# Kernel optimization log

Hardware: AMD Instinct MI355X
Metric: run time of the kernel (lower is better)

Reference implementation:

```python
import jax, jax.numpy as jnp
import numpy as np

VOCAB_SIZE = 1024
EMBED_DIM = 64
Z_SHAPE = (64, 32, 32, EMBED_DIM)


def setup_inputs() -> dict:
    key = jax.random.key(0)
    kz, kc = jax.random.split(key)
    z = jax.random.normal(kz, Z_SHAPE, dtype=jnp.float32)
    codebook = jax.random.uniform(kc, (VOCAB_SIZE, EMBED_DIM), dtype=jnp.float32)
    return {"z": z, "codebook": codebook}


def reference(z, codebook):
    # Flatten all leading dims: [N, D]
    z_flat = jnp.reshape(z, (-1, EMBED_DIM))
    # Squared euclidean distance via expansion: |z|^2 + |c|^2 - 2 z.c
    d1 = jnp.sum(z_flat ** 2, axis=1, keepdims=True)      # [N, 1]
    d2 = jnp.sum(codebook ** 2, axis=1)                   # [V]
    d3 = 2.0 * jnp.dot(z_flat, codebook.T)                # [N, V]
    distances = d1 + d2 - d3                              # [N, V]
    tokens = jnp.argmin(distances, axis=1)                # [N]
    tokens = jnp.reshape(tokens, z.shape[:-1])            # [B, H, W]
    z_quantized = codebook[tokens]                        # [B, H, W, D]
    return (z_quantized, tokens, codebook)
```

## Files before the change

### kernel.cpp

```cpp
#include <hip/hip_runtime.h>
#include <float.h>

constexpr int D     = 64;
constexpr int V     = 1024;
constexpr int NROWS = 65536;
constexpr float MARGIN = 0.01f;

typedef _Float16 half8 __attribute__((ext_vector_type(8)));
typedef float    f32x4 __attribute__((ext_vector_type(4)));

__global__ __launch_bounds__(256) void vq_prep(
    const float* __restrict__ cb, _Float16* __restrict__ wsH,
    _Float16* __restrict__ wsL, float* __restrict__ c2,
    float* __restrict__ cbout, int* __restrict__ cnt) {
  const int gid = blockIdx.x * 256 + threadIdx.x;
  if (gid == 0) cnt[0] = 0;

  ((float4*)cbout)[gid] = ((const float4*)cb)[gid];

  if (gid < V) {
    const int cw = gid;
    const float* src = cb + (size_t)cw * D;
    float part = 0.f;
#pragma unroll
    for (int chunk = 0; chunk < 8; ++chunk) {
      float4 q0 = ((const float4*)(src + chunk * 8))[0];
      float4 q1 = ((const float4*)(src + chunk * 8))[1];
      float xs[8] = {q0.x, q0.y, q0.z, q0.w, q1.x, q1.y, q1.z, q1.w};
      half8 hh, hl;
#pragma unroll
      for (int e = 0; e < 8; ++e) {
        _Float16 hi = (_Float16)xs[e];
        hh[e] = hi;
        hl[e] = (_Float16)(xs[e] - (float)hi);
        part  = fmaf(xs[e], xs[e], part);
      }
      *(half8*)&wsH[((size_t)chunk * V + cw) * 8] = hh;
      *(half8*)&wsL[((size_t)chunk * V + cw) * 8] = hl;
    }
    c2[cw] = part;
  }
}

__global__ __launch_bounds__(256, 4) void vq_screen(
    const float* __restrict__ z, const float* __restrict__ cb,
    const _Float16* __restrict__ wsH, const _Float16* __restrict__ wsL,
    const float* __restrict__ c2g,
    float* __restrict__ zq, float* __restrict__ tok,
    int* __restrict__ cnt, int* __restrict__ list) {
  __shared__ __align__(16) _Float16 sBh[8][128][8];
  __shared__ __align__(16) _Float16 sBl[8][128][8];
  __shared__ __align__(16) float sC2[128];
  __shared__ int   sW[4][16];
  __shared__ int   sFlagRows[64];
  __shared__ int   sFlagCnt, sFlagBase;

  const int tid  = threadIdx.x;
  const int lane = tid & 63;
  const int wv   = tid >> 6;
  const int l15  = lane & 15;
  const int quad = lane >> 4;
  const int gw   = blockIdx.x * 4 + wv;
  const int rowbase = gw * 16;

  if (tid == 0) sFlagCnt = 0;

  half8 afh[2], afl[2];
  {
    const float* zr = z + (size_t)(rowbase + l15) * D;
#pragma unroll
    for (int h = 0; h < 2; ++h) {
      const float4* p = (const float4*)(zr + h * 32 + quad * 8);
      float4 q0 = p[0], q1 = p[1];
      float xs[8] = {q0.x, q0.y, q0.z, q0.w, q1.x, q1.y, q1.z, q1.w};
      half8 ah, al;
#pragma unroll
      for (int e = 0; e < 8; ++e) {
        _Float16 hi = (_Float16)xs[e];
        ah[e] = hi;
        al[e] = (_Float16)(xs[e] - (float)hi);
      }
      afh[h] = ah; afl[h] = al;
    }
  }

  float b1[4], b2[4]; int i1[4];
#pragma unroll
  for (int r = 0; r < 4; ++r) { b1[r] = FLT_MAX; b2[r] = FLT_MAX; i1[r] = 0; }

  for (int phase = 0; phase < 8; ++phase) {
    __syncthreads();
#pragma unroll
    for (int i = 0; i < 8; ++i) {
      const int idx   = i * 256 + tid;
      const int seg   = idx >> 7;
      const int off   = idx & 127;
      const int chunk = seg & 7;
      const _Float16* srcb = (seg < 8) ? wsH : wsL;
      const half8 v = *(const half8*)&srcb[((size_t)chunk * V + phase * 128 + off) * 8];
      if (seg < 8) *(half8*)&sBh[chunk][off][0] = v;
      else         *(half8*)&sBl[chunk][off][0] = v;
    }
    if (tid < 32) {
      float4 q = ((const float4*)(c2g + phase * 128))[tid];
      *(float4*)&sC2[tid * 4] = q;
    }
    __syncthreads();
#pragma unroll 2
    for (int tl = 0; tl < 8; ++tl) {
      const int cwl  = tl * 16 + l15;
      const int vcol = phase * 128 + cwl;
      const float c2v = sC2[cwl];
      half8 bh0 = *(const half8*)&sBh[quad][cwl][0];
      half8 bh1 = *(const half8*)&sBh[4 + quad][cwl][0];
      half8 bl0 = *(const half8*)&sBl[quad][cwl][0];
      half8 bl1 = *(const half8*)&sBl[4 + quad][cwl][0];
      f32x4 acc = {0.f, 0.f, 0.f, 0.f};
      acc = __builtin_amdgcn_mfma_f32_16x16x32_f16(afh[0], bh0, acc, 0, 0, 0);
      acc = __builtin_amdgcn_mfma_f32_16x16x32_f16(afh[1], bh1, acc, 0, 0, 0);
      acc = __builtin_amdgcn_mfma_f32_16x16x32_f16(afh[0], bl0, acc, 0, 0, 0);
      acc = __builtin_amdgcn_mfma_f32_16x16x32_f16(afh[1], bl1, acc, 0, 0, 0);
      acc = __builtin_amdgcn_mfma_f32_16x16x32_f16(afl[0], bh0, acc, 0, 0, 0);
      acc = __builtin_amdgcn_mfma_f32_16x16x32_f16(afl[1], bh1, acc, 0, 0, 0);
#pragma unroll
      for (int r = 0; r < 4; ++r) {
        float m0 = fmaf(-2.f, acc[r], c2v);
        bool  c0 = m0 < b1[r];
        b2[r] = fminf(b2[r], fmaxf(m0, b1[r]));
        b1[r] = c0 ? m0 : b1[r];
        i1[r] = c0 ? vcol : i1[r];
      }
    }
  }

#pragma unroll
  for (int r = 0; r < 4; ++r) {
    float v1 = b1[r], v2 = b2[r]; int ix = i1[r];
#pragma unroll
    for (int s = 1; s < 16; s <<= 1) {
      float ov1 = __shfl_xor(v1, s);
      float ov2 = __shfl_xor(v2, s);
      int   oix = __shfl_xor(ix, s);
      bool take = (ov1 < v1) || (ov1 == v1 && oix < ix);
      float worse = take ? v1 : ov1;
      v2 = fminf(fminf(v2, ov2), worse);
      v1 = take ? ov1 : v1;
      ix = take ? oix : ix;
    }
    b1[r] = v1; b2[r] = v2; i1[r] = ix;
  }

  if (l15 == 0) {
#pragma unroll
    for (int r = 0; r < 4; ++r) {
      int rl = quad * 4 + r;
      sW[wv][rl] = i1[r];
      if (b2[r] - b1[r] < MARGIN) {
        int s = atomicAdd(&sFlagCnt, 1);
        sFlagRows[s] = rowbase + rl;
      }
    }
  }
  __syncthreads();
  if (tid == 0 && sFlagCnt > 0) sFlagBase = atomicAdd(cnt, sFlagCnt);
  __syncthreads();
  if (tid < sFlagCnt) list[sFlagBase + tid] = sFlagRows[tid];

  if (tid < 64) tok[blockIdx.x * 64 + tid] = (float)sW[tid >> 4][tid & 15];

#pragma unroll
  for (int i = 0; i < 4; ++i) {
    int cid = i * 256 + tid;
    int r = cid >> 4, seg = cid & 15;
    int widx = sW[r >> 4][r & 15];
    float4 val = *(const float4*)(cb + (size_t)widx * D + seg * 4);
    *(float4*)(zq + (size_t)(blockIdx.x * 64 + r) * D + seg * 4) = val;
  }
}

__global__ __launch_bounds__(256) void vq_fallback(
    const float* __restrict__ z, const float* __restrict__ cb,
    const int* __restrict__ cnt, const int* __restrict__ list,
    float* __restrict__ zq, float* __restrict__ tok) {
  __shared__ float sv[256];
  __shared__ int   si[256];
  const int t = threadIdx.x;
  const int n = cnt[0];
  for (int it = blockIdx.x; it < n; it += gridDim.x) {
    int row = __builtin_amdgcn_readfirstlane(list[it]);
    const float* zr = z + (size_t)row * D;
    float zreg[D];
#pragma unroll
    for (int i = 0; i < D / 4; ++i) {
      float4 q = ((const float4*)zr)[i];
      zreg[4 * i] = q.x; zreg[4 * i + 1] = q.y; zreg[4 * i + 2] = q.z; zreg[4 * i + 3] = q.w;
    }
    float d1 = 0.f;
#pragma unroll
    for (int i = 0; i < D; ++i) d1 = fmaf(zreg[i], zreg[i], d1);
    float best = FLT_MAX; int bidx = 0;
    for (int c = 0; c < 4; ++c) {
      int v = t + 256 * c;
      const float* cp = cb + (size_t)v * D;
      float acc = 0.f, cc = 0.f;
#pragma unroll
      for (int dd = 0; dd < D; ++dd) {
        acc = fmaf(zreg[dd], cp[dd], acc);
        cc  = fmaf(cp[dd], cp[dd], cc);
      }
      float dist = (d1 + cc) - 2.f * acc;
      if (dist < best) { best = dist; bidx = v; }
    }
    sv[t] = best; si[t] = bidx;
    __syncthreads();
    for (int s = 128; s > 0; s >>= 1) {
      if (t < s) {
        float v2 = sv[t + s]; int i2 = si[t + s];
        if (v2 < sv[t] || (v2 == sv[t] && i2 < si[t])) { sv[t] = v2; si[t] = i2; }
      }
      __syncthreads();
    }
    int win = si[0];
    if (t == 0) tok[row] = (float)win;
    if (t < 16) {
      float4 q = ((const float4*)(cb + (size_t)win * D))[t];
      ((float4*)(zq + (size_t)row * D))[t] = q;
    }
    __syncthreads();
  }
}

extern "C" void kernel_launch(void* const* d_in, const int* in_sizes, int n_in,
                              void* d_out, int out_size, void* d_ws, size_t ws_size,
                              hipStream_t stream) {
  const float* z  = (const float*)d_in[0];
  const float* cb = (const float*)d_in[1];

  float* out = (float*)d_out;
  float* zq  = out;
  float* tok = out + (size_t)NROWS * D;
  float* cbo = tok + NROWS;

  char* wsb = (char*)d_ws;
  _Float16* wsH  = (_Float16*)(wsb + 0);
  _Float16* wsL  = (_Float16*)(wsb + 131072);
  float*    c2   = (float*)(wsb + 262144);
  int*      cnt  = (int*)(wsb + 266240);
  int*      list = (int*)(wsb + 266496);

  vq_prep<<<64, 256, 0, stream>>>(cb, wsH, wsL, c2, cbo, cnt);
  vq_screen<<<1024, 256, 0, stream>>>(z, cb, wsH, wsL, c2, zq, tok, cnt, list);
  vq_fallback<<<1024, 256, 0, stream>>>(z, cb, cnt, list, zq, tok);
}
```

Baseline: 128.8 us.

## Process two 16-row tiles per wave to reuse staged codebook fragments

Each wave now handles 32 rows (two 16-row MFMA tiles) and reuses every codebook fragment loaded from shared memory for both tiles. The grid is halved to 512 blocks. This halves the global-to-LDS codebook staging and the LDS reads per row, at the cost of more registers per thread and fewer blocks to spread across the GPU.

```diff
diff --git a/kernel.cpp b/kernel.cpp
--- a/kernel.cpp
+++ b/kernel.cpp
@@ -51,8 +51,8 @@
   __shared__ __align__(16) _Float16 sBh[8][128][8];
   __shared__ __align__(16) _Float16 sBl[8][128][8];
   __shared__ __align__(16) float sC2[128];
-  __shared__ int   sW[4][16];
-  __shared__ int   sFlagRows[64];
+  __shared__ int   sW[4][32];
+  __shared__ int   sFlagRows[128];
   __shared__ int   sFlagCnt, sFlagBase;
 
   const int tid  = threadIdx.x;
@@ -61,13 +61,14 @@
   const int l15  = lane & 15;
   const int quad = lane >> 4;
   const int gw   = blockIdx.x * 4 + wv;
-  const int rowbase = gw * 16;
+  const int rowbase = gw * 32;
 
   if (tid == 0) sFlagCnt = 0;
 
-  half8 afh[2], afl[2];
-  {
-    const float* zr = z + (size_t)(rowbase + l15) * D;
+  half8 afh[2][2], afl[2][2];
+#pragma unroll
+  for (int rt = 0; rt < 2; ++rt) {
+    const float* zr = z + (size_t)(rowbase + rt * 16 + l15) * D;
 #pragma unroll
     for (int h = 0; h < 2; ++h) {
       const float4* p = (const float4*)(zr + h * 32 + quad * 8);
@@ -80,13 +81,15 @@
         ah[e] = hi;
         al[e] = (_Float16)(xs[e] - (float)hi);
       }
-      afh[h] = ah; afl[h] = al;
-    }
-  }
-
-  float b1[4], b2[4]; int i1[4];
-#pragma unroll
-  for (int r = 0; r < 4; ++r) { b1[r] = FLT_MAX; b2[r] = FLT_MAX; i1[r] = 0; }
+      afh[rt][h] = ah; afl[rt][h] = al;
+    }
+  }
+
+  float b1[2][4], b2[2][4]; int i1[2][4];
+#pragma unroll
+  for (int rt = 0; rt < 2; ++rt)
+#pragma unroll
+    for (int r = 0; r < 4; ++r) { b1[rt][r] = FLT_MAX; b2[rt][r] = FLT_MAX; i1[rt][r] = 0; }
 
   for (int phase = 0; phase < 8; ++phase) {
     __syncthreads();
@@ -115,27 +118,32 @@
       half8 bh1 = *(const half8*)&sBh[4 + quad][cwl][0];
       half8 bl0 = *(const half8*)&sBl[quad][cwl][0];
       half8 bl1 = *(const half8*)&sBl[4 + quad][cwl][0];
-      f32x4 acc = {0.f, 0.f, 0.f, 0.f};
-      acc = __builtin_amdgcn_mfma_f32_16x16x32_f16(afh[0], bh0, acc, 0, 0, 0);
-      acc = __builtin_amdgcn_mfma_f32_16x16x32_f16(afh[1], bh1, acc, 0, 0, 0);
-      acc = __builtin_amdgcn_mfma_f32_16x16x32_f16(afh[0], bl0, acc, 0, 0, 0);
-      acc = __builtin_amdgcn_mfma_f32_16x16x32_f16(afh[1], bl1, acc, 0, 0, 0);
-      acc = __builtin_amdgcn_mfma_f32_16x16x32_f16(afl[0], bh0, acc, 0, 0, 0);
-      acc = __builtin_amdgcn_mfma_f32_16x16x32_f16(afl[1], bh1, acc, 0, 0, 0);
-#pragma unroll
-      for (int r = 0; r < 4; ++r) {
-        float m0 = fmaf(-2.f, acc[r], c2v);
-        bool  c0 = m0 < b1[r];
-        b2[r] = fminf(b2[r], fmaxf(m0, b1[r]));
-        b1[r] = c0 ? m0 : b1[r];
-        i1[r] = c0 ? vcol : i1[r];
-      }
-    }
-  }
-
+#pragma unroll
+      for (int rt = 0; rt < 2; ++rt) {
+        f32x4 acc = {0.f, 0.f, 0.f, 0.f};
+        acc = __builtin_amdgcn_mfma_f32_16x16x32_f16(afh[rt][0], bh0, acc, 0, 0, 0);
+        acc = __builtin_amdgcn_mfma_f32_16x16x32_f16(afh[rt][1], bh1, acc, 0, 0, 0);
+        acc = __builtin_amdgcn_mfma_f32_16x16x32_f16(afh[rt][0], bl0, acc, 0, 0, 0);
+        acc = __builtin_amdgcn_mfma_f32_16x16x32_f16(afh[rt][1], bl1, acc, 0, 0, 0);
+        acc = __builtin_amdgcn_mfma_f32_16x16x32_f16(afl[rt][0], bh0, acc, 0, 0, 0);
+        acc = __builtin_amdgcn_mfma_f32_16x16x32_f16(afl[rt][1], bh1, acc, 0, 0, 0);
+#pragma unroll
+        for (int r = 0; r < 4; ++r) {
+          float m0 = fmaf(-2.f, acc[r], c2v);
+          bool  c0 = m0 < b1[rt][r];
+          b2[rt][r] = fminf(b2[rt][r], fmaxf(m0, b1[rt][r]));
+          b1[rt][r] = c0 ? m0 : b1[rt][r];
+          i1[rt][r] = c0 ? vcol : i1[rt][r];
+        }
+      }
+    }
+  }
+
+#pragma unroll
+  for (int rt = 0; rt < 2; ++rt)
 #pragma unroll
   for (int r = 0; r < 4; ++r) {
-    float v1 = b1[r], v2 = b2[r]; int ix = i1[r];
+    float v1 = b1[rt][r], v2 = b2[rt][r]; int ix = i1[rt][r];
 #pragma unroll
     for (int s = 1; s < 16; s <<= 1) {
       float ov1 = __shfl_xor(v1, s);
@@ -147,15 +155,17 @@
       v1 = take ? ov1 : v1;
       ix = take ? oix : ix;
     }
-    b1[r] = v1; b2[r] = v2; i1[r] = ix;
+    b1[rt][r] = v1; b2[rt][r] = v2; i1[rt][r] = ix;
   }
 
   if (l15 == 0) {
 #pragma unroll
+    for (int rt = 0; rt < 2; ++rt)
+#pragma unroll
     for (int r = 0; r < 4; ++r) {
-      int rl = quad * 4 + r;
-      sW[wv][rl] = i1[r];
-      if (b2[r] - b1[r] < MARGIN) {
+      int rl = rt * 16 + quad * 4 + r;
+      sW[wv][rl] = i1[rt][r];
+      if (b2[rt][r] - b1[rt][r] < MARGIN) {
         int s = atomicAdd(&sFlagCnt, 1);
         sFlagRows[s] = rowbase + rl;
       }
@@ -166,15 +176,15 @@
   __syncthreads();
   if (tid < sFlagCnt) list[sFlagBase + tid] = sFlagRows[tid];
 
-  if (tid < 64) tok[blockIdx.x * 64 + tid] = (float)sW[tid >> 4][tid & 15];
-
-#pragma unroll
-  for (int i = 0; i < 4; ++i) {
+  if (tid < 128) tok[blockIdx.x * 128 + tid] = (float)sW[tid >> 5][tid & 31];
+
+#pragma unroll
+  for (int i = 0; i < 8; ++i) {
     int cid = i * 256 + tid;
     int r = cid >> 4, seg = cid & 15;
-    int widx = sW[r >> 4][r & 15];
+    int widx = sW[r >> 5][r & 31];
     float4 val = *(const float4*)(cb + (size_t)widx * D + seg * 4);
-    *(float4*)(zq + (size_t)(blockIdx.x * 64 + r) * D + seg * 4) = val;
+    *(float4*)(zq + (size_t)(blockIdx.x * 128 + r) * D + seg * 4) = val;
   }
 }
 
@@ -249,6 +259,6 @@
   int*      list = (int*)(wsb + 266496);
 
   vq_prep<<<64, 256, 0, stream>>>(cb, wsH, wsL, c2, cbo, cnt);
-  vq_screen<<<1024, 256, 0, stream>>>(z, cb, wsH, wsL, c2, zq, tok, cnt, list);
+  vq_screen<<<512, 256, 0, stream>>>(z, cb, wsH, wsL, c2, zq, tok, cnt, list);
   vq_fallback<<<1024, 256, 0, stream>>>(z, cb, cnt, list, zq, tok);
 }
```

Result: slower. 132.3 us (+2.7%).

## Prefetch next codebook phase into registers while computing current phase

Applied to the files above, without the earlier changes.

Codebook half-precision tiles for the next phase are now loaded from global memory into registers before the MFMA loop of the current phase and written to LDS afterwards, so the global load latency is hidden behind compute. All codebook squared norms are also loaded into LDS once up front instead of per phase. This costs 8 extra half8 registers per thread, which may pressure occupancy under the 4-block launch bound, and adds 4KB LDS.

```diff
diff --git a/kernel.cpp b/kernel.cpp
--- a/kernel.cpp
+++ b/kernel.cpp
@@ -50,7 +50,7 @@
     int* __restrict__ cnt, int* __restrict__ list) {
   __shared__ __align__(16) _Float16 sBh[8][128][8];
   __shared__ __align__(16) _Float16 sBl[8][128][8];
-  __shared__ __align__(16) float sC2[128];
+  __shared__ __align__(16) float sC2a[1024];
   __shared__ int   sW[4][16];
   __shared__ int   sFlagRows[64];
   __shared__ int   sFlagCnt, sFlagBase;
@@ -88,29 +88,41 @@
 #pragma unroll
   for (int r = 0; r < 4; ++r) { b1[r] = FLT_MAX; b2[r] = FLT_MAX; i1[r] = 0; }
 
+  {
+    float4 qc = ((const float4*)c2g)[tid];
+    *(float4*)&sC2a[tid * 4] = qc;
+  }
+#pragma unroll
+  for (int i = 0; i < 8; ++i) {
+    const int idx   = i * 256 + tid;
+    const int seg   = idx >> 7;
+    const int off   = idx & 127;
+    const int chunk = seg & 7;
+    const _Float16* srcb = (seg < 8) ? wsH : wsL;
+    const half8 v = *(const half8*)&srcb[((size_t)chunk * V + off) * 8];
+    if (seg < 8) *(half8*)&sBh[chunk][off][0] = v;
+    else         *(half8*)&sBl[chunk][off][0] = v;
+  }
+  __syncthreads();
+
   for (int phase = 0; phase < 8; ++phase) {
-    __syncthreads();
-#pragma unroll
-    for (int i = 0; i < 8; ++i) {
-      const int idx   = i * 256 + tid;
-      const int seg   = idx >> 7;
-      const int off   = idx & 127;
-      const int chunk = seg & 7;
-      const _Float16* srcb = (seg < 8) ? wsH : wsL;
-      const half8 v = *(const half8*)&srcb[((size_t)chunk * V + phase * 128 + off) * 8];
-      if (seg < 8) *(half8*)&sBh[chunk][off][0] = v;
-      else         *(half8*)&sBl[chunk][off][0] = v;
-    }
-    if (tid < 32) {
-      float4 q = ((const float4*)(c2g + phase * 128))[tid];
-      *(float4*)&sC2[tid * 4] = q;
-    }
-    __syncthreads();
+    half8 pre[8];
+    if (phase < 7) {
+#pragma unroll
+      for (int i = 0; i < 8; ++i) {
+        const int idx   = i * 256 + tid;
+        const int seg   = idx >> 7;
+        const int off   = idx & 127;
+        const int chunk = seg & 7;
+        const _Float16* srcb = (seg < 8) ? wsH : wsL;
+        pre[i] = *(const half8*)&srcb[((size_t)chunk * V + (phase + 1) * 128 + off) * 8];
+      }
+    }
 #pragma unroll 2
     for (int tl = 0; tl < 8; ++tl) {
       const int cwl  = tl * 16 + l15;
       const int vcol = phase * 128 + cwl;
-      const float c2v = sC2[cwl];
+      const float c2v = sC2a[phase * 128 + cwl];
       half8 bh0 = *(const half8*)&sBh[quad][cwl][0];
       half8 bh1 = *(const half8*)&sBh[4 + quad][cwl][0];
       half8 bl0 = *(const half8*)&sBl[quad][cwl][0];
@@ -130,6 +142,19 @@
         b1[r] = c0 ? m0 : b1[r];
         i1[r] = c0 ? vcol : i1[r];
       }
+    }
+    __syncthreads();
+    if (phase < 7) {
+#pragma unroll
+      for (int i = 0; i < 8; ++i) {
+        const int idx   = i * 256 + tid;
+        const int seg   = idx >> 7;
+        const int off   = idx & 127;
+        const int chunk = seg & 7;
+        if (seg < 8) *(half8*)&sBh[chunk][off][0] = pre[i];
+        else         *(half8*)&sBl[chunk][off][0] = pre[i];
+      }
+      __syncthreads();
     }
   }
 
```

Result: no change. 130.6 us (+1.4%).
